# Performance work log

Measured on AMD Instinct MI355X. Metric: run time of the kernel, lower is better.

## Reference

```python
import jax, jax.numpy as jnp
import numpy as np

B, P, G = 64, 512, 64      # batch of independent nets, populations, generator inputs
N = P + G                   # presynaptic channels per population
H = 32                      # neuron-MLP hidden width
DT = 0.1                    # integration step (ms)
EREV_MIN, EREV_MAX = -75.0, 0.0


def setup_inputs() -> dict:
    key = jax.random.key(0)
    ks = jax.random.split(key, 16)
    state = jax.random.uniform(ks[0], (B, P), dtype=jnp.float32)          # prev firing rates
    inp = jax.random.uniform(ks[1], (B, G), dtype=jnp.float32)            # generator rates
    R = jnp.ones((B, P, N), dtype=jnp.float32)                            # recovered resources
    U = jnp.zeros((B, P, N), dtype=jnp.float32)                           # utilization
    A = jnp.zeros((B, P, N), dtype=jnp.float32)                           # active resources
    gsyn_max = 2.0 * jax.random.uniform(ks[2], (P, N), dtype=jnp.float32)
    pconn = jax.random.uniform(ks[3], (P, N), dtype=jnp.float32)
    Uinc = 0.1 + 0.5 * jax.random.uniform(ks[4], (P, N), dtype=jnp.float32)
    tau_r = 100.0 + 400.0 * jax.random.uniform(ks[5], (P, N), dtype=jnp.float32)  # recovery (ms)
    tau_f = 10.0 + 50.0 * jax.random.uniform(ks[6], (P, N), dtype=jnp.float32)    # facilitation
    tau_d = 2.0 + 5.0 * jax.random.uniform(ks[7], (P, N), dtype=jnp.float32)      # decay
    Erev = jnp.where(jax.random.uniform(ks[8], (P, N)) > 0.5, 0.0, -75.0).astype(jnp.float32)
    mask = jnp.ones((P, N), dtype=bool)                                   # is_connected_mask
    Cm = 0.5 + 2.0 * jax.random.uniform(ks[9], (P,), dtype=jnp.float32)
    W1 = 0.5 * jax.random.normal(ks[10], (P, 2, H), dtype=jnp.float32)
    b1 = 0.5 * jax.random.normal(ks[11], (P, H), dtype=jnp.float32)
    W2 = 0.5 * jax.random.normal(ks[12], (P, H, 1), dtype=jnp.float32)
    b2 = 0.5 * jax.random.normal(ks[13], (P, 1), dtype=jnp.float32)
    return {"state": state, "inp": inp, "R": R, "U": U, "A": A,
            "gsyn_max": gsyn_max, "pconn": pconn, "Uinc": Uinc,
            "tau_r": tau_r, "tau_f": tau_f, "tau_d": tau_d,
            "Erev": Erev, "mask": mask, "Cm": Cm,
            "W1": W1, "b1": b1, "W2": W2, "b2": b2}


def reference(state, inp, R, U, A, gsyn_max, pconn, Uinc, tau_r, tau_f, tau_d,
              Erev, mask, Cm, W1, b1, W2, b2):
    # --- TimeStepLayer.call: concat prev state with generator input -> full presyn vector
    x = jnp.concatenate([state, inp], axis=-1)                  # [B, N]
    SR = x[:, None, :] * pconn                                  # [B, P, N] spike prob per conn

    # --- TsodycsMarkramSynapse one Euler step (all populations fused)
    e_d = jnp.exp(-DT / tau_d)
    e_r = jnp.exp(-DT / tau_r)
    e_f = jnp.exp(-DT / tau_f)
    tau1r = jnp.where(tau_d != tau_r, tau_d / (tau_d - tau_r), 1e-13)
    a_dec = A * e_d
    r_dec = 1.0 + (R - 1.0 + tau1r * U) * e_r - tau1r * U
    u_dec = U * e_f
    u0 = u_dec + Uinc * (1.0 - u_dec) * SR                      # new utilization
    a0 = a_dec + u0 * r_dec * SR                                # new active fraction

    # --- synaptic drive features per population
    g = gsyn_max * a0 * mask                                    # [B, P, N]
    g_tot = jnp.sum(g, axis=-1)                                 # [B, P]
    E_eff = jnp.sum(g * Erev, axis=-1) / (g_tot + 1e-8)
    E_norm = (E_eff - EREV_MIN) / (EREV_MAX - EREV_MIN)
    g_norm = g_tot / (g_tot + Cm[None, :])
    feat = jnp.stack([E_norm, g_norm], axis=-1)                 # [B, P, 2]

    # --- frozen per-population neuron net (square activation, sigmoid rate)
    h = jnp.square(jnp.einsum('bpf,pfh->bph', feat, W1) + b1)   # [B, P, H]
    out = jax.nn.sigmoid(jnp.einsum('bph,pho->bpo', h, W2) + b2)[..., 0]  # [B, P]
    return out
```

## Files before the change

kernel.cpp:

```cpp
#include <hip/hip_runtime.h>

#define PP 512
#define GG 64
#define NN 576

#define DERIVE(i, PC, UI, TR, TF, TD, GS, ER)                                \
  {                                                                          \
    float e_r  = __expf(-0.1f * __builtin_amdgcn_rcpf(TR));                  \
    float e_f  = __expf(-0.1f * __builtin_amdgcn_rcpf(TF));                  \
    float e_d  = __expf(-0.1f * __builtin_amdgcn_rcpf(TD));                  \
    float diff = (TD) - (TR);                                                \
    float t1r  = (diff != 0.0f) ? (TD) * __builtin_amdgcn_rcpf(diff)         \
                                : 1e-13f;                                    \
    pcg[i] = (PC) * (GS);                                                    \
    up[i]  = (UI) * (PC);                                                    \
    ef[i]  = e_f;                                                            \
    er[i]  = e_r;                                                            \
    c1[i]  = t1r * (e_r - 1.0f);                                             \
    ged[i] = (GS) * e_d;                                                     \
    Ev[i]  = (ER);                                                           \
  }

#define STEP(i, Rv, Uv, Av, Xv)                                              \
  {                                                                          \
    float srg  = (Xv) * pcg[i];                                              \
    float udec = (Uv) * ef[i];                                               \
    float upx  = up[i] * (Xv);                                               \
    float u0   = udec + upx * (1.0f - udec);                                 \
    float rdec = 1.0f + ((Rv) - 1.0f) * er[i] + c1[i] * (Uv);                \
    float cg   = fmaf(ged[i], (Av), srg * u0 * rdec);                        \
    gt += cg;                                                                \
    ge = fmaf(Ev[i], cg, ge);                                                \
  }

#define COMPUTE(RW, bb)                                                      \
  {                                                                          \
    float gt = 0.0f, ge = 0.0f;                                              \
    STEP(0, (RW).r0.x, (RW).u0.x, (RW).a0.x, (RW).x0.x)                      \
    STEP(1, (RW).r0.y, (RW).u0.y, (RW).a0.y, (RW).x0.y)                      \
    STEP(2, (RW).r0.z, (RW).u0.z, (RW).a0.z, (RW).x0.z)                      \
    STEP(3, (RW).r0.w, (RW).u0.w, (RW).a0.w, (RW).x0.w)                      \
    STEP(4, (RW).r1.x, (RW).u1.x, (RW).a1.x, (RW).x1.x)                      \
    STEP(5, (RW).r1.y, (RW).u1.y, (RW).a1.y, (RW).x1.y)                      \
    STEP(6, (RW).r1.z, (RW).u1.z, (RW).a1.z, (RW).x1.z)                      \
    STEP(7, (RW).r1.w, (RW).u1.w, (RW).a1.w, (RW).x1.w)                      \
    STEP(8, (RW).rt, (RW).ut, (RW).at, (RW).xt)                              \
    _Pragma("unroll")                                                        \
    for (int m = 32; m >= 1; m >>= 1) {                                      \
        gt += __shfl_xor(gt, m, 64);                                         \
        ge += __shfl_xor(ge, m, 64);                                         \
    }                                                                        \
    float Eeff = ge / (gt + 1e-8f);                                          \
    float En   = (Eeff + 75.0f) / 75.0f;                                     \
    float gn   = gt / (gt + cmp);                                            \
    float pre  = fmaf(En, w1a, fmaf(gn, w1b, b1j));                          \
    float hv   = pre * pre;                                                  \
    float v    = hv * w2j;                                                   \
    _Pragma("unroll")                                                        \
    for (int m = 16; m >= 1; m >>= 1) v += __shfl_xor(v, m, 64);             \
    float s = v + b2p;                                                       \
    float r = 1.0f / (1.0f + __expf(-s));                                    \
    if (lane == 0) out[(size_t)(bb) * PP + p] = r;                           \
  }

#define SBAR __builtin_amdgcn_sched_barrier(0)

struct Row {
    float4 r0, r1, u0, u1, a0, a1, x0, x1;
    float  rt, ut, at, xt;
};

__device__ __forceinline__ Row load_row(const float* __restrict__ R,
                                        const float* __restrict__ U,
                                        const float* __restrict__ A,
                                        const float* __restrict__ state,
                                        const float* __restrict__ inp,
                                        int b, int p, int lane)
{
    Row rw;
    const size_t rbase = ((size_t)b * PP + p) * (size_t)NN;
    const size_t r4    = rbase >> 2;
    const int    s4    = (b * PP) >> 2;
    rw.r0 = ((const float4*)R)[r4 + lane];
    rw.u0 = ((const float4*)U)[r4 + lane];
    rw.a0 = ((const float4*)A)[r4 + lane];
    rw.x0 = ((const float4*)state)[s4 + lane];
    rw.r1 = ((const float4*)R)[r4 + 64 + lane];
    rw.u1 = ((const float4*)U)[r4 + 64 + lane];
    rw.a1 = ((const float4*)A)[r4 + 64 + lane];
    rw.x1 = ((const float4*)state)[s4 + 64 + lane];
    const size_t o = rbase + 512 + (size_t)lane;
    rw.rt = R[o];
    rw.ut = U[o];
    rw.at = A[o];
    rw.xt = inp[b * GG + lane];
    return rw;
}

__global__ __launch_bounds__(256, 3)
void timestep_kernel(const float* __restrict__ state,
                     const float* __restrict__ inp,
                     const float* __restrict__ R,
                     const float* __restrict__ U,
                     const float* __restrict__ A,
                     const float* __restrict__ gsyn_max,
                     const float* __restrict__ pconn,
                     const float* __restrict__ Uinc,
                     const float* __restrict__ tau_r,
                     const float* __restrict__ tau_f,
                     const float* __restrict__ tau_d,
                     const float* __restrict__ Erev,
                     const float* __restrict__ Cm,
                     const float* __restrict__ W1,
                     const float* __restrict__ b1,
                     const float* __restrict__ W2,
                     const float* __restrict__ b2,
                     float* __restrict__ out)
{
    const int tid  = threadIdx.x;
    const int lane = tid & 63;
    const int wave = tid >> 6;
    const int p    = blockIdx.x >> 2;
    const int qtr  = blockIdx.x & 3;

    float pcg[9], up[9], ef[9], er[9], c1[9], ged[9], Ev[9];

    const int prow = p * NN;
    #pragma unroll
    for (int c = 0; c < 2; ++c) {
        const int f4 = (prow >> 2) + c * 64 + lane;
        float4 v_pc = ((const float4*)pconn)[f4];
        float4 v_ui = ((const float4*)Uinc)[f4];
        float4 v_tr = ((const float4*)tau_r)[f4];
        float4 v_tf = ((const float4*)tau_f)[f4];
        float4 v_td = ((const float4*)tau_d)[f4];
        float4 v_gs = ((const float4*)gsyn_max)[f4];
        float4 v_er = ((const float4*)Erev)[f4];
        DERIVE(c * 4 + 0, v_pc.x, v_ui.x, v_tr.x, v_tf.x, v_td.x, v_gs.x, v_er.x)
        DERIVE(c * 4 + 1, v_pc.y, v_ui.y, v_tr.y, v_tf.y, v_td.y, v_gs.y, v_er.y)
        DERIVE(c * 4 + 2, v_pc.z, v_ui.z, v_tr.z, v_tf.z, v_td.z, v_gs.z, v_er.z)
        DERIVE(c * 4 + 3, v_pc.w, v_ui.w, v_tr.w, v_tf.w, v_td.w, v_gs.w, v_er.w)
    }
    {
        const int o = prow + 512 + lane;
        DERIVE(8, pconn[o], Uinc[o], tau_r[o], tau_f[o], tau_d[o],
               gsyn_max[o], Erev[o])
    }

    const int   j   = lane & 31;
    const float w1a = W1[p * 64 + j];
    const float w1b = W1[p * 64 + 32 + j];
    const float b1j = b1[p * 32 + j];
    const float w2j = W2[p * 32 + j];
    const float b2p = b2[p];
    const float cmp = Cm[p];

    const int b0 = qtr * 16 + wave;

    Row rA = load_row(R, U, A, state, inp, b0,      p, lane);
    Row rB = load_row(R, U, A, state, inp, b0 + 4,  p, lane);
    SBAR;
    COMPUTE(rA, b0)
    rA = load_row(R, U, A, state, inp, b0 + 8,  p, lane);
    SBAR;
    COMPUTE(rB, b0 + 4)
    rB = load_row(R, U, A, state, inp, b0 + 12, p, lane);
    SBAR;
    COMPUTE(rA, b0 + 8)
    COMPUTE(rB, b0 + 12)
}

extern "C" void kernel_launch(void* const* d_in, const int* in_sizes, int n_in,
                              void* d_out, int out_size, void* d_ws, size_t ws_size,
                              hipStream_t stream) {
    const float* state = (const float*)d_in[0];
    const float* inp   = (const float*)d_in[1];
    const float* R     = (const float*)d_in[2];
    const float* U     = (const float*)d_in[3];
    const float* A     = (const float*)d_in[4];
    const float* gsyn  = (const float*)d_in[5];
    const float* pconn = (const float*)d_in[6];
    const float* Uinc  = (const float*)d_in[7];
    const float* taur  = (const float*)d_in[8];
    const float* tauf  = (const float*)d_in[9];
    const float* taud  = (const float*)d_in[10];
    const float* Erev  = (const float*)d_in[11];
    const float* Cm    = (const float*)d_in[13];
    const float* W1    = (const float*)d_in[14];
    const float* b1    = (const float*)d_in[15];
    const float* W2    = (const float*)d_in[16];
    const float* b2    = (const float*)d_in[17];
    float* out = (float*)d_out;

    hipLaunchKernelGGL(timestep_kernel, dim3(2048), dim3(256), 0, stream,
                       state, inp, R, U, A, gsyn, pconn, Uinc, taur, tauf, taud,
                       Erev, Cm, W1, b1, W2, b2, out);
}
```

Before: 256.1 us.

## Derive per-population synapse params once per block into LDS and read from shared memory

Instead of every wave loading and deriving the seven per-channel parameter arrays (exp, rcp) into registers, wave 0 computes them once and stores them to LDS, and all waves read them from there after a barrier. The batch loop becomes a plain loop without explicit double-buffered prefetch, with the batch order rotated per block, and launch bounds are raised to 4 blocks/CU. This removes redundant transcendental work and register pressure to raise occupancy. In exchange it adds a block barrier where waves 1-3 sit idle during the derive, plus extra LDS traffic, and drops the manual load/compute overlap.

```diff
diff --git a/kernel.cpp b/kernel.cpp
--- a/kernel.cpp
+++ b/kernel.cpp
@@ -4,7 +4,9 @@
 #define GG 64
 #define NN 576
 
-#define DERIVE(i, PC, UI, TR, TF, TD, GS, ER)                                \
+#define PA(a, ch) lds_par[(a) * NN + (ch)]
+
+#define DERIVE1(PC, UI, TR, TF, TD, GS, ER, Dpcg, Dup, Def, Der, Dc1, Dged, DEv) \
   {                                                                          \
     float e_r  = __expf(-0.1f * __builtin_amdgcn_rcpf(TR));                  \
     float e_f  = __expf(-0.1f * __builtin_amdgcn_rcpf(TF));                  \
@@ -12,92 +14,48 @@
     float diff = (TD) - (TR);                                                \
     float t1r  = (diff != 0.0f) ? (TD) * __builtin_amdgcn_rcpf(diff)         \
                                 : 1e-13f;                                    \
-    pcg[i] = (PC) * (GS);                                                    \
-    up[i]  = (UI) * (PC);                                                    \
-    ef[i]  = e_f;                                                            \
-    er[i]  = e_r;                                                            \
-    c1[i]  = t1r * (e_r - 1.0f);                                             \
-    ged[i] = (GS) * e_d;                                                     \
-    Ev[i]  = (ER);                                                           \
+    Dpcg = (PC) * (GS);                                                      \
+    Dup  = (UI) * (PC);                                                      \
+    Def  = e_f;                                                              \
+    Der  = e_r;                                                              \
+    Dc1  = t1r * (e_r - 1.0f);                                               \
+    Dged = (GS) * e_d;                                                       \
+    DEv  = (ER);                                                             \
   }
 
-#define STEP(i, Rv, Uv, Av, Xv)                                              \
+#define STEPQ(Vpcg, Vup, Vef, Ver, Vc1, Vged, VEv, Rv, Uv, Av, Xv)           \
   {                                                                          \
-    float srg  = (Xv) * pcg[i];                                              \
-    float udec = (Uv) * ef[i];                                               \
-    float upx  = up[i] * (Xv);                                               \
+    float srg  = (Xv) * (Vpcg);                                              \
+    float udec = (Uv) * (Vef);                                               \
+    float upx  = (Vup) * (Xv);                                               \
     float u0   = udec + upx * (1.0f - udec);                                 \
-    float rdec = 1.0f + ((Rv) - 1.0f) * er[i] + c1[i] * (Uv);                \
-    float cg   = fmaf(ged[i], (Av), srg * u0 * rdec);                        \
+    float rdec = 1.0f + ((Rv) - 1.0f) * (Ver) + (Vc1) * (Uv);                \
+    float cg   = fmaf((Vged), (Av), srg * u0 * rdec);                        \
     gt += cg;                                                                \
-    ge = fmaf(Ev[i], cg, ge);                                                \
+    ge = fmaf((VEv), cg, ge);                                                \
   }
 
-#define COMPUTE(RW, bb)                                                      \
+#define CHUNK(c, RV, UV, AV, XV)                                             \
   {                                                                          \
-    float gt = 0.0f, ge = 0.0f;                                              \
-    STEP(0, (RW).r0.x, (RW).u0.x, (RW).a0.x, (RW).x0.x)                      \
-    STEP(1, (RW).r0.y, (RW).u0.y, (RW).a0.y, (RW).x0.y)                      \
-    STEP(2, (RW).r0.z, (RW).u0.z, (RW).a0.z, (RW).x0.z)                      \
-    STEP(3, (RW).r0.w, (RW).u0.w, (RW).a0.w, (RW).x0.w)                      \
-    STEP(4, (RW).r1.x, (RW).u1.x, (RW).a1.x, (RW).x1.x)                      \
-    STEP(5, (RW).r1.y, (RW).u1.y, (RW).a1.y, (RW).x1.y)                      \
-    STEP(6, (RW).r1.z, (RW).u1.z, (RW).a1.z, (RW).x1.z)                      \
-    STEP(7, (RW).r1.w, (RW).u1.w, (RW).a1.w, (RW).x1.w)                      \
-    STEP(8, (RW).rt, (RW).ut, (RW).at, (RW).xt)                              \
-    _Pragma("unroll")                                                        \
-    for (int m = 32; m >= 1; m >>= 1) {                                      \
-        gt += __shfl_xor(gt, m, 64);                                         \
-        ge += __shfl_xor(ge, m, 64);                                         \
-    }                                                                        \
-    float Eeff = ge / (gt + 1e-8f);                                          \
-    float En   = (Eeff + 75.0f) / 75.0f;                                     \
-    float gn   = gt / (gt + cmp);                                            \
-    float pre  = fmaf(En, w1a, fmaf(gn, w1b, b1j));                          \
-    float hv   = pre * pre;                                                  \
-    float v    = hv * w2j;                                                   \
-    _Pragma("unroll")                                                        \
-    for (int m = 16; m >= 1; m >>= 1) v += __shfl_xor(v, m, 64);             \
-    float s = v + b2p;                                                       \
-    float r = 1.0f / (1.0f + __expf(-s));                                    \
-    if (lane == 0) out[(size_t)(bb) * PP + p] = r;                           \
+    const int ch = (c) * 256 + 4 * lane;                                     \
+    float4 Qpcg = *(const float4*)&PA(0, ch);                                \
+    float4 Qup  = *(const float4*)&PA(1, ch);                                \
+    float4 Qef  = *(const float4*)&PA(2, ch);                                \
+    float4 Qer  = *(const float4*)&PA(3, ch);                                \
+    float4 Qc1  = *(const float4*)&PA(4, ch);                                \
+    float4 Qged = *(const float4*)&PA(5, ch);                                \
+    float4 QEv  = *(const float4*)&PA(6, ch);                                \
+    STEPQ(Qpcg.x, Qup.x, Qef.x, Qer.x, Qc1.x, Qged.x, QEv.x,                 \
+          (RV).x, (UV).x, (AV).x, (XV).x)                                    \
+    STEPQ(Qpcg.y, Qup.y, Qef.y, Qer.y, Qc1.y, Qged.y, QEv.y,                 \
+          (RV).y, (UV).y, (AV).y, (XV).y)                                    \
+    STEPQ(Qpcg.z, Qup.z, Qef.z, Qer.z, Qc1.z, Qged.z, QEv.z,                 \
+          (RV).z, (UV).z, (AV).z, (XV).z)                                    \
+    STEPQ(Qpcg.w, Qup.w, Qef.w, Qer.w, Qc1.w, Qged.w, QEv.w,                 \
+          (RV).w, (UV).w, (AV).w, (XV).w)                                    \
   }
 
-#define SBAR __builtin_amdgcn_sched_barrier(0)
-
-struct Row {
-    float4 r0, r1, u0, u1, a0, a1, x0, x1;
-    float  rt, ut, at, xt;
-};
-
-__device__ __forceinline__ Row load_row(const float* __restrict__ R,
-                                        const float* __restrict__ U,
-                                        const float* __restrict__ A,
-                                        const float* __restrict__ state,
-                                        const float* __restrict__ inp,
-                                        int b, int p, int lane)
-{
-    Row rw;
-    const size_t rbase = ((size_t)b * PP + p) * (size_t)NN;
-    const size_t r4    = rbase >> 2;
-    const int    s4    = (b * PP) >> 2;
-    rw.r0 = ((const float4*)R)[r4 + lane];
-    rw.u0 = ((const float4*)U)[r4 + lane];
-    rw.a0 = ((const float4*)A)[r4 + lane];
-    rw.x0 = ((const float4*)state)[s4 + lane];
-    rw.r1 = ((const float4*)R)[r4 + 64 + lane];
-    rw.u1 = ((const float4*)U)[r4 + 64 + lane];
-    rw.a1 = ((const float4*)A)[r4 + 64 + lane];
-    rw.x1 = ((const float4*)state)[s4 + 64 + lane];
-    const size_t o = rbase + 512 + (size_t)lane;
-    rw.rt = R[o];
-    rw.ut = U[o];
-    rw.at = A[o];
-    rw.xt = inp[b * GG + lane];
-    return rw;
-}
-
-__global__ __launch_bounds__(256, 3)
+__global__ __launch_bounds__(256, 4)
 void timestep_kernel(const float* __restrict__ state,
                      const float* __restrict__ inp,
                      const float* __restrict__ R,
@@ -117,34 +75,55 @@
                      const float* __restrict__ b2,
                      float* __restrict__ out)
 {
+    __shared__ float lds_par[7 * NN];
+
     const int tid  = threadIdx.x;
     const int lane = tid & 63;
     const int wave = tid >> 6;
     const int p    = blockIdx.x >> 2;
     const int qtr  = blockIdx.x & 3;
 
-    float pcg[9], up[9], ef[9], er[9], c1[9], ged[9], Ev[9];
-
-    const int prow = p * NN;
-    #pragma unroll
-    for (int c = 0; c < 2; ++c) {
-        const int f4 = (prow >> 2) + c * 64 + lane;
-        float4 v_pc = ((const float4*)pconn)[f4];
-        float4 v_ui = ((const float4*)Uinc)[f4];
-        float4 v_tr = ((const float4*)tau_r)[f4];
-        float4 v_tf = ((const float4*)tau_f)[f4];
-        float4 v_td = ((const float4*)tau_d)[f4];
-        float4 v_gs = ((const float4*)gsyn_max)[f4];
-        float4 v_er = ((const float4*)Erev)[f4];
-        DERIVE(c * 4 + 0, v_pc.x, v_ui.x, v_tr.x, v_tf.x, v_td.x, v_gs.x, v_er.x)
-        DERIVE(c * 4 + 1, v_pc.y, v_ui.y, v_tr.y, v_tf.y, v_td.y, v_gs.y, v_er.y)
-        DERIVE(c * 4 + 2, v_pc.z, v_ui.z, v_tr.z, v_tf.z, v_td.z, v_gs.z, v_er.z)
-        DERIVE(c * 4 + 3, v_pc.w, v_ui.w, v_tr.w, v_tf.w, v_td.w, v_gs.w, v_er.w)
-    }
-    {
-        const int o = prow + 512 + lane;
-        DERIVE(8, pconn[o], Uinc[o], tau_r[o], tau_f[o], tau_d[o],
-               gsyn_max[o], Erev[o])
+    if (wave == 0) {
+        const int prow = p * NN;
+        #pragma unroll
+        for (int c = 0; c < 2; ++c) {
+            const int f4 = (prow >> 2) + c * 64 + lane;
+            float4 v_pc = ((const float4*)pconn)[f4];
+            float4 v_ui = ((const float4*)Uinc)[f4];
+            float4 v_tr = ((const float4*)tau_r)[f4];
+            float4 v_tf = ((const float4*)tau_f)[f4];
+            float4 v_td = ((const float4*)tau_d)[f4];
+            float4 v_gs = ((const float4*)gsyn_max)[f4];
+            float4 v_er = ((const float4*)Erev)[f4];
+            float4 Dpcg, Dup, Def, Der, Dc1, Dged, DEv;
+            DERIVE1(v_pc.x, v_ui.x, v_tr.x, v_tf.x, v_td.x, v_gs.x, v_er.x,
+                    Dpcg.x, Dup.x, Def.x, Der.x, Dc1.x, Dged.x, DEv.x)
+            DERIVE1(v_pc.y, v_ui.y, v_tr.y, v_tf.y, v_td.y, v_gs.y, v_er.y,
+                    Dpcg.y, Dup.y, Def.y, Der.y, Dc1.y, Dged.y, DEv.y)
+            DERIVE1(v_pc.z, v_ui.z, v_tr.z, v_tf.z, v_td.z, v_gs.z, v_er.z,
+                    Dpcg.z, Dup.z, Def.z, Der.z, Dc1.z, Dged.z, DEv.z)
+            DERIVE1(v_pc.w, v_ui.w, v_tr.w, v_tf.w, v_td.w, v_gs.w, v_er.w,
+                    Dpcg.w, Dup.w, Def.w, Der.w, Dc1.w, Dged.w, DEv.w)
+            const int ch = c * 256 + 4 * lane;
+            *(float4*)&PA(0, ch) = Dpcg;
+            *(float4*)&PA(1, ch) = Dup;
+            *(float4*)&PA(2, ch) = Def;
+            *(float4*)&PA(3, ch) = Der;
+            *(float4*)&PA(4, ch) = Dc1;
+            *(float4*)&PA(5, ch) = Dged;
+            *(float4*)&PA(6, ch) = DEv;
+        }
+        {
+            const int o = prow + 512 + lane;
+            float Dpcg, Dup, Def, Der, Dc1, Dged, DEv;
+            DERIVE1(pconn[o], Uinc[o], tau_r[o], tau_f[o], tau_d[o],
+                    gsyn_max[o], Erev[o],
+                    Dpcg, Dup, Def, Der, Dc1, Dged, DEv)
+            const int ch = 512 + lane;
+            PA(0, ch) = Dpcg;  PA(1, ch) = Dup;  PA(2, ch) = Def;
+            PA(3, ch) = Der;   PA(4, ch) = Dc1;  PA(5, ch) = Dged;
+            PA(6, ch) = DEv;
+        }
     }
 
     const int   j   = lane & 31;
@@ -155,19 +134,58 @@
     const float b2p = b2[p];
     const float cmp = Cm[p];
 
-    const int b0 = qtr * 16 + wave;
-
-    Row rA = load_row(R, U, A, state, inp, b0,      p, lane);
-    Row rB = load_row(R, U, A, state, inp, b0 + 4,  p, lane);
-    SBAR;
-    COMPUTE(rA, b0)
-    rA = load_row(R, U, A, state, inp, b0 + 8,  p, lane);
-    SBAR;
-    COMPUTE(rB, b0 + 4)
-    rB = load_row(R, U, A, state, inp, b0 + 12, p, lane);
-    SBAR;
-    COMPUTE(rA, b0 + 8)
-    COMPUTE(rB, b0 + 12)
+    __syncthreads();
+
+    const int rot = (blockIdx.x >> 2) & 3;
+    for (int t = 0; t < 4; ++t) {
+        const int i = (t + rot) & 3;
+        const int b = qtr * 16 + wave + 4 * i;
+
+        const size_t rbase = ((size_t)b * PP + p) * (size_t)NN;
+        const size_t r4    = rbase >> 2;
+        const int    s4    = (b * PP) >> 2;
+
+        float4 rv0 = ((const float4*)R)[r4 + lane];
+        float4 uv0 = ((const float4*)U)[r4 + lane];
+        float4 av0 = ((const float4*)A)[r4 + lane];
+        float4 xv0 = ((const float4*)state)[s4 + lane];
+        float4 rv1 = ((const float4*)R)[r4 + 64 + lane];
+        float4 uv1 = ((const float4*)U)[r4 + 64 + lane];
+        float4 av1 = ((const float4*)A)[r4 + 64 + lane];
+        float4 xv1 = ((const float4*)state)[s4 + 64 + lane];
+        const size_t o = rbase + 512 + (size_t)lane;
+        float rts = R[o];
+        float uts = U[o];
+        float ats = A[o];
+        float xts = inp[b * GG + lane];
+
+        float gt = 0.0f, ge = 0.0f;
+        CHUNK(0, rv0, uv0, av0, xv0)
+        CHUNK(1, rv1, uv1, av1, xv1)
+        {
+            const int ch = 512 + lane;
+            STEPQ(PA(0, ch), PA(1, ch), PA(2, ch), PA(3, ch), PA(4, ch),
+                  PA(5, ch), PA(6, ch), rts, uts, ats, xts)
+        }
+
+        #pragma unroll
+        for (int m = 32; m >= 1; m >>= 1) {
+            gt += __shfl_xor(gt, m, 64);
+            ge += __shfl_xor(ge, m, 64);
+        }
+
+        float Eeff = ge / (gt + 1e-8f);
+        float En   = (Eeff + 75.0f) / 75.0f;
+        float gn   = gt / (gt + cmp);
+        float pre  = fmaf(En, w1a, fmaf(gn, w1b, b1j));
+        float hv   = pre * pre;
+        float v    = hv * w2j;
+        #pragma unroll
+        for (int m = 16; m >= 1; m >>= 1) v += __shfl_xor(v, m, 64);
+        float s = v + b2p;
+        float r = 1.0f / (1.0f + __expf(-s));
+        if (lane == 0) out[(size_t)b * PP + p] = r;
+    }
 }
 
 extern "C" void kernel_launch(void* const* d_in, const int* in_sizes, int n_in,
```

Result: no change. 258.7 us (+1.0%).
